# Kernel optimization log

Measured on AMD Instinct MI355X. Metric: run time of the kernel, lower is better.

The kernel has to match this reference:

```python
import jax, jax.numpy as jnp
import numpy as np

IN_FEATURES = 256
EMBED = 512
HEADS = 8
HEAD_DIM = EMBED // HEADS
BLOCKS = 2
FFN = 2048
CLASSES = 1000
NWIRES = 8
BATCH = 8
SEQ = 2048


def _posenc(seq, dim, dtype):
    pos = jnp.arange(seq, dtype=jnp.float32)[:, None]
    div = jnp.exp(jnp.arange(0, dim, 2, dtype=jnp.float32) * (-jnp.log(10000.0) / dim))
    pe = jnp.zeros((seq, dim), dtype=jnp.float32)
    pe = pe.at[:, 0::2].set(jnp.sin(pos * div))
    pe = pe.at[:, 1::2].set(jnp.cos(pos * div))
    return pe.astype(dtype)


def _layer_norm(x, g, b, eps=1e-5):
    mu = jnp.mean(x, axis=-1, keepdims=True)
    var = jnp.var(x, axis=-1, keepdims=True)
    return (x - mu) * jax.lax.rsqrt(var + eps) * g + b


def setup_inputs() -> dict:
    key = jax.random.key(0)
    ks = jax.random.split(key, 20)
    s = 0.02
    inp = {
        'x': jax.random.normal(ks[0], (BATCH, SEQ, IN_FEATURES), dtype=jnp.float32),
        'Wi': jax.random.normal(ks[1], (EMBED, IN_FEATURES), dtype=jnp.float32) * s,
        'bi': jnp.zeros((EMBED,), dtype=jnp.float32),
        'theta_a': jax.random.normal(ks[2], (BLOCKS, NWIRES), dtype=jnp.float32),
        'Wproj': jax.random.normal(ks[3], (BLOCKS, EMBED, NWIRES), dtype=jnp.float32) * s,
        'Wq': jax.random.normal(ks[4], (BLOCKS, EMBED, EMBED), dtype=jnp.float32) * s,
        'Wk': jax.random.normal(ks[5], (BLOCKS, EMBED, EMBED), dtype=jnp.float32) * s,
        'Wv': jax.random.normal(ks[6], (BLOCKS, EMBED, EMBED), dtype=jnp.float32) * s,
        'Wo': jax.random.normal(ks[7], (BLOCKS, EMBED, EMBED), dtype=jnp.float32) * s,
        'g1': jnp.ones((BLOCKS, EMBED), dtype=jnp.float32),
        'b1': jnp.zeros((BLOCKS, EMBED), dtype=jnp.float32),
        'phi': jax.random.normal(ks[8], (BLOCKS, NWIRES), dtype=jnp.float32),
        'W1': jax.random.normal(ks[9], (BLOCKS, FFN, NWIRES), dtype=jnp.float32) * s,
        'W2': jax.random.normal(ks[10], (BLOCKS, EMBED, FFN), dtype=jnp.float32) * s,
        'g2': jnp.ones((BLOCKS, EMBED), dtype=jnp.float32),
        'b2': jnp.zeros((BLOCKS, EMBED), dtype=jnp.float32),
        'Wc': jax.random.normal(ks[11], (CLASSES, EMBED), dtype=jnp.float32) * s,
        'bc': jnp.zeros((CLASSES,), dtype=jnp.float32),
    }
    return inp


def reference(x, Wi, bi, theta_a, Wproj, Wq, Wk, Wv, Wo, g1, b1, phi, W1, W2, g2, b2, Wc, bc):
    b, s, _ = x.shape
    h = jnp.einsum('bsf,ef->bse', x, Wi) + bi          # input_proj
    h = h + _posenc(s, EMBED, h.dtype)[None]           # positional encoding
    scale = 1.0 / np.sqrt(HEAD_DIM)
    for l in range(BLOCKS):
        # --- quantum attention sublayer ---
        # RX encode first NWIRES features + trainable RX per wire -> <Z> = cos(x + theta)
        q_out = jnp.cos(h[..., :NWIRES] + theta_a[l])  # [b,s,nw]
        x_q = jnp.einsum('bsw,ew->bse', q_out, Wproj[l])
        q = jnp.einsum('bse,fe->bsf', x_q, Wq[l]).reshape(b, s, HEADS, HEAD_DIM).transpose(0, 2, 1, 3)
        k = jnp.einsum('bse,fe->bsf', x_q, Wk[l]).reshape(b, s, HEADS, HEAD_DIM).transpose(0, 2, 1, 3)
        v = jnp.einsum('bse,fe->bsf', x_q, Wv[l]).reshape(b, s, HEADS, HEAD_DIM).transpose(0, 2, 1, 3)
        scores = jnp.einsum('bhqd,bhkd->bhqk', q, k) * scale
        attn = jax.nn.softmax(scores, axis=-1)
        out = jnp.einsum('bhqk,bhkd->bhqd', attn, v)
        out = out.transpose(0, 2, 1, 3).reshape(b, s, EMBED)
        attn_out = jnp.einsum('bse,fe->bsf', out, Wo[l])
        h = _layer_norm(h + attn_out, g1[l], b1[l])
        # --- quantum feed-forward sublayer ---
        # RY encode + trainable RY per wire -> <Z> = cos(x + phi)
        qf = jnp.cos(h[..., :NWIRES] + phi[l])         # [b,s,nw]
        f = jnp.einsum('bsw,fw->bsf', qf, W1[l])       # nw -> ffn
        f = jnp.einsum('bsf,ef->bse', jax.nn.relu(f), W2[l])
        h = _layer_norm(h + f, g2[l], b2[l])
    pooled = jnp.mean(h, axis=1)                        # [b, embed]
    logits = jnp.einsum('be,ce->bc', pooled, Wc) + bc
    return logits
```

## Files before the change

### kernel.cpp

```cpp
#include <hip/hip_runtime.h>
#include <hip/hip_bf16.h>
#include <math.h>

#define B_   8
#define S_   2048
#define T_   (B_*S_)
#define FIN  256
#define E_   512
#define H_   8
#define D_   64
#define FFN_ 2048
#define NC_  1000
#define NW_  8

typedef __attribute__((ext_vector_type(8))) short short8;
typedef __attribute__((ext_vector_type(4))) short short4v;
typedef __attribute__((ext_vector_type(4))) float f32x4;
typedef __attribute__((ext_vector_type(2))) unsigned int uint2v;
typedef __attribute__((ext_vector_type(4))) unsigned int uint4v;

__device__ __forceinline__ unsigned short f2bf(float f) {
    __hip_bfloat16 h = __float2bfloat16(f);
    return __builtin_bit_cast(unsigned short, h);
}
__device__ __forceinline__ float bf2f(unsigned short u) {
    return __builtin_bit_cast(float, (unsigned int)u << 16);
}

__device__ __forceinline__ unsigned cvtpk_bf16(float lo, float hi) {
    unsigned r;
    asm("v_cvt_pk_bf16_f32 %0, %1, %2" : "=v"(r) : "v"(lo), "v"(hi));
    return r;
}

#if defined(__has_builtin)
#if __has_builtin(__builtin_amdgcn_permlane32_swap) && __has_builtin(__builtin_amdgcn_permlane16_swap)
#define HAVE_PLSWAP 1
#endif
#endif

__device__ __forceinline__ void lswap32(unsigned &a, unsigned &b) {
#if defined(HAVE_PLSWAP)
    uint2v t = __builtin_amdgcn_permlane32_swap(a, b, false, false);
    a = t[0]; b = t[1];
#else
    unsigned as = (unsigned)__shfl_xor((int)a, 32);
    unsigned bs = (unsigned)__shfl_xor((int)b, 32);
    bool hi = (threadIdx.x & 32) != 0;
    unsigned na = hi ? bs : a;
    unsigned nb = hi ? b  : as;
    a = na; b = nb;
#endif
}
__device__ __forceinline__ void lswap16(unsigned &a, unsigned &b) {
#if defined(HAVE_PLSWAP)
    uint2v t = __builtin_amdgcn_permlane16_swap(a, b, false, false);
    a = t[0]; b = t[1];
#else
    unsigned as = (unsigned)__shfl_xor((int)a, 16);
    unsigned bs = (unsigned)__shfl_xor((int)b, 16);
    bool hi = (threadIdx.x & 16) != 0;
    unsigned na = hi ? bs : a;
    unsigned nb = hi ? b  : as;
    a = na; b = nb;
#endif
}

__device__ __forceinline__ void gld16(void* l, const void* g) {
    __builtin_amdgcn_global_load_lds(
        (const __attribute__((address_space(1))) unsigned int*)g,
        (__attribute__((address_space(3))) unsigned int*)l,
        16, 0, 0);
}

#if defined(__has_builtin)
#if __has_builtin(__builtin_amdgcn_mfma_f32_16x16x16bf16_1k)
#define HAVE_MFMA16 1
#endif
#endif

__device__ __forceinline__ f32x4 mfma16(short4v a, short4v b, f32x4 c) {
#ifdef HAVE_MFMA16
    return __builtin_amdgcn_mfma_f32_16x16x16bf16_1k(a, b, c, 0, 0, 0);
#else
    short8 a8 = {a[0], a[1], a[2], a[3], 0, 0, 0, 0};
    short8 b8 = {b[0], b[1], b[2], b[3], 0, 0, 0, 0};
    return __builtin_amdgcn_mfma_f32_16x16x32_bf16(a8, b8, c, 0, 0, 0);
#endif
}

__global__ __launch_bounds__(256)
void cvt_all(const float* __restrict__ x,  const float* __restrict__ Wi,
             const float* __restrict__ Wo, const float* __restrict__ W2,
             const float* __restrict__ W1,
             unsigned short* xb, unsigned short* Wib,
             unsigned short* Wob, unsigned short* W2b, unsigned short* W1b)
{
    int g = blockIdx.x*256 + threadIdx.x;
    const float* s; unsigned short* d; int o;
    if      (g < 1048576) { s = x;  d = xb;  o = g; }
    else if (g < 1081344) { s = Wi; d = Wib; o = g - 1048576; }
    else if (g < 1212416) { s = Wo; d = Wob; o = g - 1081344; }
    else if (g < 1736704) { s = W2; d = W2b; o = g - 1212416; }
    else                  { s = W1; d = W1b; o = g - 1736704; }
    float4 vv = ((const float4*)s)[o];
    ushort4 u;
    u.x = f2bf(vv.x); u.y = f2bf(vv.y); u.z = f2bf(vv.z); u.w = f2bf(vv.w);
    ((ushort4*)d)[o] = u;
}

__global__ __launch_bounds__(64)
void weff_kernel(const float* __restrict__ Wq, const float* __restrict__ Wk,
                 const float* __restrict__ Wv, const float* __restrict__ Wproj,
                 unsigned short* __restrict__ Weff)
{
    const int f = blockIdx.x, l = blockIdx.y, which = blockIdx.z;
    const int lane = threadIdx.x;
    const float* W = (which == 0 ? Wq : which == 1 ? Wk : Wv)
                     + (size_t)l*E_*E_ + (size_t)f*E_;
    const float* P = Wproj + (size_t)l*E_*NW_;
    const int wv = lane & 7;
    float s = 0.f;
    for (int e = (lane >> 3)*64; e < (lane >> 3)*64 + 64; e++)
        s += W[e] * P[e*NW_ + wv];
    #pragma unroll
    for (int off = 8; off < 64; off <<= 1) s += __shfl_xor(s, off);
    const float scale = (which == 0) ? 0.18033688011112042f : 1.f;
    if (lane < 8)
        Weff[((size_t)(which*2 + l)*E_ + f)*NW_ + lane] = f2bf(s * scale);
}

__global__ __launch_bounds__(64)
void gram_kernel(const unsigned short* __restrict__ Weff, unsigned short* __restrict__ G)
{
    const int hh = blockIdx.x, l = blockIdx.y;
    const int lane = threadIdx.x;
    const int w = lane >> 3, wp = lane & 7;
    const unsigned short* Wq_e = Weff + (size_t)(0*2 + l)*E_*NW_ + (size_t)hh*64*NW_;
    const unsigned short* Wk_e = Weff + (size_t)(1*2 + l)*E_*NW_ + (size_t)hh*64*NW_;
    float s = 0.f;
    for (int d = 0; d < 64; d++)
        s += bf2f(Wq_e[d*NW_ + w]) * bf2f(Wk_e[d*NW_ + wp]);
    G[(size_t)(l*8 + hh)*64 + w*8 + wp] = f2bf(s);
}

__global__ __launch_bounds__(64)
void wov_kernel(const float* __restrict__ Wo, const unsigned short* __restrict__ Weff,
                unsigned short* __restrict__ WoV)
{
    const int f = blockIdx.x, l = blockIdx.y;
    const int lane = threadIdx.x;
    const int hh = lane >> 3, w = lane & 7;
    const float* wrow = Wo + (size_t)l*E_*E_ + (size_t)f*E_ + hh*64;
    const unsigned short* Wv_e = Weff + (size_t)(2*2 + l)*E_*NW_ + (size_t)hh*64*NW_;
    float s = 0.f;
    for (int d = 0; d < 64; d++)
        s += wrow[d] * bf2f(Wv_e[d*NW_ + w]);
    WoV[(size_t)(l*E_ + f)*64 + lane] = f2bf(s);
}

__global__ __launch_bounds__(256)
void qc_small(const unsigned short* __restrict__ h, const float* __restrict__ theta,
              const unsigned short* __restrict__ G,
              unsigned short* __restrict__ c8, unsigned short* __restrict__ c8T,
              unsigned short* __restrict__ gkb)
{
    const int tid = threadIdx.x;
    const int t0 = blockIdx.x * 32;
    __shared__ float cs[32][8];
    __shared__ float Gs[512];
    {
        int tl = tid >> 3, wv2 = tid & 7;
        cs[tl][wv2] = cosf(bf2f(h[(size_t)(t0 + tl)*E_ + wv2]) + theta[wv2]);
        Gs[tid]       = bf2f(G[tid]);
        Gs[tid + 256] = bf2f(G[tid + 256]);
    }
    __syncthreads();
    const int tl = tid >> 3, hh = tid & 7;
    const int bb = (t0 + tl) >> 11, ss = (t0 + tl) & (S_ - 1);
    float c[8];
    #pragma unroll
    for (int i = 0; i < 8; i++) c[i] = cs[tl][i];
    unsigned short u[8] __attribute__((aligned(16)));
    #pragma unroll
    for (int w = 0; w < 8; w++) {
        float s = 0.f;
        #pragma unroll
        for (int wp = 0; wp < 8; wp++) s += Gs[hh*64 + w*8 + wp] * c[wp];
        u[w] = f2bf(s);
    }
    *(float4*)&gkb[((size_t)(bb*H_ + hh)*S_ + ss)*8] = *(float4*)u;
    if (tid < 32) {
        unsigned short v[8] __attribute__((aligned(16)));
        #pragma unroll
        for (int i = 0; i < 8; i++) v[i] = f2bf(cs[tid][i]);
        *(float4*)&c8[(size_t)(t0 + tid)*8] = *(float4*)v;
    } else if (tid < 40) {
        int w = tid - 32;
        unsigned short v[32] __attribute__((aligned(16)));
        #pragma unroll
        for (int s = 0; s < 32; s++) v[s] = f2bf(cs[s][w]);
        unsigned short* dst = c8T + ((size_t)(t0 >> 11)*8 + w)*S_ + (t0 & (S_ - 1));
        #pragma unroll
        for (int cq = 0; cq < 4; cq++) *(float4*)(dst + cq*8) = *(float4*)&v[cq*8];
    }
}

template<int TC_BF16, int MODE>
__global__ __launch_bounds__(256)
void gemm_mfma(const unsigned short* __restrict__ A,
               const unsigned short* __restrict__ Bm,
               void* __restrict__ Cv, int M, int N, int K,
               float scale, const float* __restrict__ bias)
{
    __shared__ char Lraw[32768];
    unsigned short* Al = (unsigned short*)Lraw;
    unsigned short* Bl = (unsigned short*)(Lraw + 16384);
    float* Ot = (float*)Lraw;

    const int tid  = threadIdx.x;
    const int lane = tid & 63;
    const int w    = tid >> 6;
    const int wx   = w & 1, wy = w >> 1;
    int bx, by;
    {
        int nx = gridDim.x;
        int bid = blockIdx.y * nx + blockIdx.x;
        int rpx = gridDim.y >> 3;
        int xcd = bid & 7, idx = bid >> 3;
        by = xcd * rpx + idx / nx;
        bx = idx % nx;
    }
    const int rowBase = by * 128;
    const int colBase = bx * 128;
    const int l15  = lane & 15;
    const int quad = lane >> 4;
    const int srow = lane >> 2;
    const int gch  = (lane & 3) ^ ((srow >> 1) & 3);
    const int swz  = (l15 >> 1) & 3;

    f32x4 acc[4][4] = {};

    #pragma unroll
    for (int it = 0; it < 2; it++) {
        int rb = it*64 + w*16;
        gld16(&Al[rb*32], A  + (size_t)(rowBase + rb + srow)*K + gch*8);
        gld16(&Bl[rb*32], Bm + (size_t)(colBase + rb + srow)*K + gch*8);
    }

    for (int k0 = 0; k0 < K; k0 += 32) {
        const int cur = (k0 >> 5) & 1;
        __syncthreads();
        if (k0 + 32 < K) {
            #pragma unroll
            for (int it = 0; it < 2; it++) {
                int rb = it*64 + w*16;
                gld16(&Al[(1-cur)*4096 + rb*32], A  + (size_t)(rowBase + rb + srow)*K + k0 + 32 + gch*8);
                gld16(&Bl[(1-cur)*4096 + rb*32], Bm + (size_t)(colBase + rb + srow)*K + k0 + 32 + gch*8);
            }
        }
        short8 af[4], bfr[4];
        #pragma unroll
        for (int mi = 0; mi < 4; mi++)
            af[mi] = *(const short8*)&Al[cur*4096 + (wy*64 + mi*16 + l15)*32 + ((quad ^ swz) << 3)];
        #pragma unroll
        for (int ni = 0; ni < 4; ni++)
            bfr[ni] = *(const short8*)&Bl[cur*4096 + (wx*64 + ni*16 + l15)*32 + ((quad ^ swz) << 3)];
        #pragma unroll
        for (int mi = 0; mi < 4; mi++)
            #pragma unroll
            for (int ni = 0; ni < 4; ni++)
                acc[mi][ni] = __builtin_amdgcn_mfma_f32_16x16x32_bf16(
                    af[mi], bfr[ni], acc[mi][ni], 0, 0, 0);
    }

    #pragma unroll
    for (int mi = 0; mi < 4; mi++) {
        __syncthreads();
        #pragma unroll
        for (int ni = 0; ni < 4; ni++) {
            #pragma unroll
            for (int r = 0; r < 4; r++) {
                float v = acc[mi][ni][r] * scale;
                if (MODE == 1) {
                    int row = rowBase + wy*64 + mi*16 + quad*4 + r;
                    int col = colBase + wx*64 + ni*16 + l15;
                    int s = row & (S_ - 1);
                    float freq = __expf(-0.017988946039244957f * (float)(col & ~1));
                    float ang = (float)s * freq;
                    v += bias[col] + ((col & 1) ? cosf(ang) : sinf(ang));
                }
                Ot[(wy*16 + quad*4 + r)*132 + wx*64 + ni*16 + l15] = v;
            }
        }
        __syncthreads();
        {
            int rl = tid >> 3, c0 = (tid & 7) * 16;
            int grow = rowBase + (rl >> 4)*64 + mi*16 + (rl & 15);
            float vv[16];
            #pragma unroll
            for (int j = 0; j < 4; j++)
                *(float4*)&vv[j*4] = *(const float4*)&Ot[rl*132 + c0 + j*4];
            if (TC_BF16) {
                unsigned short u[16] __attribute__((aligned(16)));
                #pragma unroll
                for (int i = 0; i < 16; i++) u[i] = f2bf(vv[i]);
                unsigned short* dst = (unsigned short*)Cv + (size_t)grow*N + colBase + c0;
                *(float4*)dst       = *(float4*)&u[0];
                *(float4*)(dst + 8) = *(float4*)&u[8];
            } else {
                float* dst = (float*)Cv + (size_t)grow*N + colBase + c0;
                #pragma unroll
                for (int j = 0; j < 4; j++)
                    *(float4*)(dst + j*4) = *(const float4*)&vv[j*4];
            }
        }
    }
}

__global__ __launch_bounds__(256)
void gemm_w2f(const unsigned short* __restrict__ h, const float* __restrict__ phi,
              const unsigned short* __restrict__ W1b,
              const unsigned short* __restrict__ W2b,
              unsigned short* __restrict__ tmp)
{
    __shared__ char Lraw[17408];
    unsigned short* Wl = (unsigned short*)Lraw;
    float* Ot = (float*)Lraw;

    const int tid  = threadIdx.x;
    const int lane = tid & 63;
    const int w    = tid >> 6;
    const int tx   = w & 1, ty = w >> 1;
    const int l15  = lane & 15;
    const int quad = lane >> 4;
    const int srow = lane >> 2;
    const int gch  = (lane & 3) ^ ((srow >> 1) & 3);
    const int swz  = (l15 >> 1) & 3;

    const int bid = blockIdx.x;
    const int xcd = bid & 7;
    const int eb  = xcd >> 1;
    const int tb  = (xcd & 1) * 64 + (bid >> 3);
    const int tBase = tb * 128;
    const int eBase = eb * 128;

    short4v cosfr[4];
    #pragma unroll
    for (int nt = 0; nt < 4; nt++) {
        short4v c = {0,0,0,0};
        if (quad < 2) {
            int tok = tBase + ty*64 + nt*16 + l15;
            #pragma unroll
            for (int i = 0; i < 4; i++) {
                int wv = quad*4 + i;
                c[i] = (short)f2bf(cosf(bf2f(h[(size_t)tok*E_ + wv]) + phi[wv]));
            }
        }
        cosfr[nt] = c;
    }

    #pragma unroll
    for (int it = 0; it < 2; it++) {
        int rb = w*32 + it*16;
        gld16(&Wl[rb*32], W2b + (size_t)(eBase + rb + srow)*FFN_ + gch*8);
    }

    const f32x4 fzero = {0.f, 0.f, 0.f, 0.f};
    short4v w1fA[2] = {{0,0,0,0},{0,0,0,0}};

    auto ffn1_pack = [&](short8* pfr_out) {
        unsigned Pm[4][4];
        #pragma unroll
        for (int nt = 0; nt < 4; nt++) {
            #pragma unroll
            for (int jb = 0; jb < 2; jb++) {
                f32x4 c = mfma16(w1fA[jb], cosfr[nt], fzero);
                Pm[nt][jb*2]   = cvtpk_bf16(fmaxf(c[0], 0.f), fmaxf(c[1], 0.f));
                Pm[nt][jb*2+1] = cvtpk_bf16(fmaxf(c[2], 0.f), fmaxf(c[3], 0.f));
            }
            lswap32(Pm[nt][0], Pm[nt][2]); lswap32(Pm[nt][1], Pm[nt][3]);
            lswap16(Pm[nt][0], Pm[nt][2]); lswap16(Pm[nt][1], Pm[nt][3]);
            uint4v u = { Pm[nt][0], Pm[nt][1], Pm[nt][2], Pm[nt][3] };
            pfr_out[nt] = __builtin_bit_cast(short8, u);
        }
    };
    auto load_w1f = [&](int k0) {
        #pragma unroll
        for (int jb = 0; jb < 2; jb++)
            if (quad < 2)
                w1fA[jb] = *(const short4v*)&W1b[(size_t)(k0 + jb*16 + l15)*NW_ + quad*4];
    };

    load_w1f(0);
    short8 pf_cur[4], pf_next[4];
    ffn1_pack(pf_cur);
    load_w1f(32);

    f32x4 acc[4][4] = {};

    for (int k0 = 0; k0 < FFN_; k0 += 32) {
        const int cur = (k0 >> 5) & 1;
        __syncthreads();
        if (k0 + 32 < FFN_) {
            #pragma unroll
            for (int it = 0; it < 2; it++) {
                int rb = w*32 + it*16;
                gld16(&Wl[(1-cur)*4096 + rb*32],
                      W2b + (size_t)(eBase + rb + srow)*FFN_ + k0 + 32 + gch*8);
            }
            ffn1_pack(pf_next);
            if (k0 + 64 < FFN_) load_w1f(k0 + 64);
        }
        #pragma unroll
        for (int et = 0; et < 4; et++) {
            short8 wf = *(const short8*)&Wl[cur*4096 + (tx*64 + et*16 + l15)*32
                                             + ((quad ^ swz) << 3)];
            #pragma unroll
            for (int nt = 0; nt < 4; nt++)
                acc[et][nt] = __builtin_amdgcn_mfma_f32_16x16x32_bf16(
                    wf, pf_cur[nt], acc[et][nt], 0, 0, 0);
        }
        #pragma unroll
        for (int nt = 0; nt < 4; nt++) pf_cur[nt] = pf_next[nt];
    }

    #pragma unroll
    for (int et = 0; et < 4; et++) {
        __syncthreads();
        #pragma unroll
        for (int nt = 0; nt < 4; nt++)
            #pragma unroll
            for (int r = 0; r < 4; r++)
                Ot[(ty*64 + nt*16 + l15)*33 + tx*16 + quad*4 + r] = acc[et][nt][r];
        __syncthreads();
        int token = tid >> 1, half = tid & 1;
        unsigned short u[16] __attribute__((aligned(16)));
        #pragma unroll
        for (int i = 0; i < 16; i++) u[i] = f2bf(Ot[token*33 + half*16 + i]);
        unsigned short* dst = tmp + (size_t)(tBase + token)*E_ + eBase + half*64 + et*16;
        *(float4*)dst       = *(float4*)&u[0];
        *(float4*)(dst + 8) = *(float4*)&u[8];
    }
}

__global__ __launch_bounds__(256)
void flash_q(const unsigned short* __restrict__ c8,
             const unsigned short* __restrict__ c8T,
             const unsigned short* __restrict__ gkb,
             unsigned short* __restrict__ yout)
{
    const int tid  = threadIdx.x;
    const int lane = tid & 63;
    const int wv   = tid >> 6;
    const int l15  = lane & 15;
    const int quad = lane >> 4;
    const int bid  = blockIdx.x;
    const int xcd  = bid & 7;
    const int rest = bid >> 3;
    const int combo = xcd * 8 + (rest >> 4);
    const int qt = rest & 15;
    const int hh = combo & 7;
    const int bb = combo >> 3;
    const size_t qrow0 = (size_t)bb*S_ + (size_t)qt*128;
    const unsigned short* gkp  = gkb + (size_t)(bb*H_ + hh)*S_*NW_;
    const unsigned short* c8Tp = c8T + (size_t)bb*8*S_;

    short4v cqfr[2] = {{0,0,0,0},{0,0,0,0}};
    if (quad < 2) {
        #pragma unroll
        for (int mi = 0; mi < 2; mi++)
            cqfr[mi] = *(const short4v*)&c8[(qrow0 + wv*32 + mi*16 + l15)*NW_ + quad*4];
    }
    const short8 ones8 = {(short)0x3F80, (short)0x3F80, (short)0x3F80, (short)0x3F80,
                          (short)0x3F80, (short)0x3F80, (short)0x3F80, (short)0x3F80};
    f32x4 y[2] = {};

    for (int kt = 0; kt < S_/64; kt++) {
        f32x4 Sc[2][4] = {};
        #pragma unroll
        for (int nt = 0; nt < 4; nt++) {
            short4v gkf = {0,0,0,0};
            if (quad < 2)
                gkf = *(const short4v*)&gkp[(size_t)(kt*64 + nt*16 + l15)*NW_ + quad*4];
            Sc[0][nt] = mfma16(gkf, cqfr[0], Sc[0][nt]);
            Sc[1][nt] = mfma16(gkf, cqfr[1], Sc[1][nt]);
        }
        unsigned Pm[2][8];
        #pragma unroll
        for (int mi = 0; mi < 2; mi++)
            #pragma unroll
            for (int nt = 0; nt < 4; nt++) {
                float e0 = __builtin_amdgcn_exp2f(Sc[mi][nt][0]);
                float e1 = __builtin_amdgcn_exp2f(Sc[mi][nt][1]);
                float e2 = __builtin_amdgcn_exp2f(Sc[mi][nt][2]);
                float e3 = __builtin_amdgcn_exp2f(Sc[mi][nt][3]);
                Pm[mi][nt*2]   = cvtpk_bf16(e0, e1);
                Pm[mi][nt*2+1] = cvtpk_bf16(e2, e3);
            }
        #pragma unroll
        for (int mi = 0; mi < 2; mi++) {
            lswap32(Pm[mi][0], Pm[mi][2]); lswap32(Pm[mi][1], Pm[mi][3]);
            lswap32(Pm[mi][4], Pm[mi][6]); lswap32(Pm[mi][5], Pm[mi][7]);
            lswap16(Pm[mi][0], Pm[mi][2]); lswap16(Pm[mi][1], Pm[mi][3]);
            lswap16(Pm[mi][4], Pm[mi][6]); lswap16(Pm[mi][5], Pm[mi][7]);
        }
        short8 pf[2][2];
        #pragma unroll
        for (int mi = 0; mi < 2; mi++)
            #pragma unroll
            for (int kb = 0; kb < 2; kb++) {
                uint4v u = { Pm[mi][kb*4], Pm[mi][kb*4+1], Pm[mi][kb*4+2], Pm[mi][kb*4+3] };
                pf[mi][kb] = __builtin_bit_cast(short8, u);
            }
        #pragma unroll
        for (int kb = 0; kb < 2; kb++) {
            short8 a8 = {0,0,0,0,0,0,0,0};
            if (l15 < 8)
                a8 = *(const short8*)&c8Tp[(size_t)l15*S_ + kt*64 + kb*32 + quad*8];
            else if (l15 == 8)
                a8 = ones8;
            y[0] = __builtin_amdgcn_mfma_f32_16x16x32_bf16(a8, pf[0][kb], y[0], 0, 0, 0);
            y[1] = __builtin_amdgcn_mfma_f32_16x16x32_bf16(a8, pf[1][kb], y[1], 0, 0, 0);
        }
    }

    #pragma unroll
    for (int mi = 0; mi < 2; mi++) {
        float rs = __shfl(y[mi][0], 32 + l15);
        float inv = 1.f / rs;
        if (quad < 2) {
            unsigned d0 = cvtpk_bf16(y[mi][0]*inv, y[mi][1]*inv);
            unsigned d1 = cvtpk_bf16(y[mi][2]*inv, y[mi][3]*inv);
            unsigned* dst = (unsigned*)&yout[(qrow0 + wv*32 + mi*16 + l15)*64 + hh*8 + quad*4];
            dst[0] = d0; dst[1] = d1;
        }
    }
}

__global__ __launch_bounds__(256)
void add_ln(unsigned short* __restrict__ h, const unsigned short* __restrict__ delta,
            const float* __restrict__ g, const float* __restrict__ b)
{
    const int lane = threadIdx.x & 63;
    const int t = blockIdx.x*4 + (threadIdx.x >> 6);
    const size_t base = (size_t)t*E_ + lane*8;
    uint4 hv = *(const uint4*)&h[base];
    uint4 dv = *(const uint4*)&delta[base];
    float x[8];
    #pragma unroll
    for (int i = 0; i < 4; i++) {
        unsigned hu = ((const unsigned*)&hv)[i], du = ((const unsigned*)&dv)[i];
        x[2*i]   = bf2f((unsigned short)(hu & 0xffff)) + bf2f((unsigned short)(du & 0xffff));
        x[2*i+1] = bf2f((unsigned short)(hu >> 16))    + bf2f((unsigned short)(du >> 16));
    }
    float s = 0.f, sq = 0.f;
    #pragma unroll
    for (int i = 0; i < 8; i++) { s += x[i]; sq += x[i]*x[i]; }
    #pragma unroll
    for (int off = 1; off < 64; off <<= 1) {
        s  += __shfl_xor(s,  off);
        sq += __shfl_xor(sq, off);
    }
    float mu  = s * (1.f/E_);
    float var = sq * (1.f/E_) - mu*mu;
    float rstd = rsqrtf(var + 1e-5f);
    float4 g0 = *(const float4*)&g[lane*8], g1 = *(const float4*)&g[lane*8 + 4];
    float4 b0 = *(const float4*)&b[lane*8], b1 = *(const float4*)&b[lane*8 + 4];
    float gg[8] = {g0.x,g0.y,g0.z,g0.w,g1.x,g1.y,g1.z,g1.w};
    float bb[8] = {b0.x,b0.y,b0.z,b0.w,b1.x,b1.y,b1.z,b1.w};
    uint4 ov;
    #pragma unroll
    for (int i = 0; i < 4; i++) {
        unsigned lo = f2bf((x[2*i]   - mu)*rstd*gg[2*i]   + bb[2*i]);
        unsigned hi = f2bf((x[2*i+1] - mu)*rstd*gg[2*i+1] + bb[2*i+1]);
        ((unsigned*)&ov)[i] = lo | (hi << 16);
    }
    *(uint4*)&h[base] = ov;
}

__global__ __launch_bounds__(256)
void pool_partial(const unsigned short* __restrict__ h, float* __restrict__ part)
{
    const int chunk = blockIdx.x, bb = blockIdx.y, tid = threadIdx.x;
    for (int e = tid; e < E_; e += 256) {
        const unsigned short* p = h + ((size_t)bb*S_ + (size_t)chunk*128)*E_ + e;
        float s = 0.f;
        for (int r = 0; r < 128; r++) s += bf2f(p[(size_t)r*E_]);
        part[(size_t)(bb*16 + chunk)*E_ + e] = s;
    }
}

__global__ __launch_bounds__(256)
void pool_final(const float* __restrict__ part, float* __restrict__ pooled)
{
    const int bb = blockIdx.x, tid = threadIdx.x;
    for (int e = tid; e < E_; e += 256) {
        float s = 0.f;
        #pragma unroll
        for (int c = 0; c < 16; c++) s += part[(size_t)(bb*16 + c)*E_ + e];
        pooled[bb*E_ + e] = s * (1.f/S_);
    }
}

__global__ __launch_bounds__(64)
void classify(const float* __restrict__ pooled, const float* __restrict__ Wc,
              const float* __restrict__ bc, float* __restrict__ out)
{
    const int c = blockIdx.x, bb = blockIdx.y, lane = threadIdx.x;
    const float* p = pooled + bb*E_;
    const float* wc = Wc + (size_t)c*E_;
    float s = 0.f;
    for (int e = lane; e < E_; e += 64) s += p[e]*wc[e];
    #pragma unroll
    for (int off = 1; off < 64; off <<= 1) s += __shfl_xor(s, off);
    if (lane == 0) out[bb*NC_ + c] = s + bc[c];
}

extern "C" void kernel_launch(void* const* d_in, const int* in_sizes, int n_in,
                              void* d_out, int out_size, void* d_ws, size_t ws_size,
                              hipStream_t stream)
{
    const float* x       = (const float*)d_in[0];
    const float* Wi      = (const float*)d_in[1];
    const float* bi      = (const float*)d_in[2];
    const float* theta_a = (const float*)d_in[3];
    const float* Wproj   = (const float*)d_in[4];
    const float* Wq      = (const float*)d_in[5];
    const float* Wk      = (const float*)d_in[6];
    const float* Wv      = (const float*)d_in[7];
    const float* Wo      = (const float*)d_in[8];
    const float* g1      = (const float*)d_in[9];
    const float* b1      = (const float*)d_in[10];
    const float* phi     = (const float*)d_in[11];
    const float* W1      = (const float*)d_in[12];
    const float* W2      = (const float*)d_in[13];
    const float* g2      = (const float*)d_in[14];
    const float* b2      = (const float*)d_in[15];
    const float* Wc      = (const float*)d_in[16];
    const float* bc      = (const float*)d_in[17];
    float* out = (float*)d_out;

    char* ws = (char*)d_ws;
    const size_t MB = 1024u*1024u;
    unsigned short* h      = (unsigned short*)(ws + 0*MB);
    unsigned short* tmp    = (unsigned short*)(ws + 16*MB);
    unsigned short* c8     = (unsigned short*)(ws + 32*MB);
    unsigned short* c8T    = (unsigned short*)(ws + 33*MB);
    unsigned short* gkb    = (unsigned short*)(ws + 34*MB);
    unsigned short* yout   = (unsigned short*)(ws + 48*MB);
    unsigned short* xb     = (unsigned short*)(ws + 96*MB);
    unsigned short* Wib    = (unsigned short*)(ws + 104*MB);
    unsigned short* Wob    = (unsigned short*)(ws + 105*MB);
    unsigned short* W2b    = (unsigned short*)(ws + 106*MB);
    unsigned short* W1b    = (unsigned short*)(ws + 110*MB);
    unsigned short* Weff   = (unsigned short*)(ws + 111*MB);
    unsigned short* Gbuf   = (unsigned short*)(ws + 111*MB + 64*1024);
    unsigned short* WoV    = (unsigned short*)(ws + 111*MB + 128*1024);
    float*          part   = (float*)(ws + 112*MB);
    float*          pooled = (float*)(ws + 112*MB + 512*1024);

    cvt_all<<<6816, 256, 0, stream>>>(x, Wi, Wo, W2, W1, xb, Wib, Wob, W2b, W1b);
    weff_kernel<<<dim3(E_, 2, 3), 64, 0, stream>>>(Wq, Wk, Wv, Wproj, Weff);
    gram_kernel<<<dim3(H_, 2), 64, 0, stream>>>(Weff, Gbuf);
    wov_kernel<<<dim3(E_, 2), 64, 0, stream>>>(Wo, Weff, WoV);

    gemm_mfma<1,1><<<dim3(E_/128, T_/128), 256, 0, stream>>>(
        xb, Wib, h, T_, E_, FIN, 1.f, bi);

    for (int l = 0; l < 2; l++) {
        qc_small<<<T_/32, 256, 0, stream>>>(h, theta_a + l*NW_, Gbuf + (size_t)l*512,
                                            c8, c8T, gkb);
        flash_q<<<(S_/128)*H_*B_, 256, 0, stream>>>(c8, c8T, gkb, yout);
        gemm_mfma<1,0><<<dim3(E_/128, T_/128), 256, 0, stream>>>(
            yout, WoV + (size_t)l*E_*64, tmp, T_, E_, 64, 1.f, nullptr);
        add_ln<<<T_/4, 256, 0, stream>>>(h, tmp, g1 + l*E_, b1 + l*E_);

        gemm_w2f<<<512, 256, 0, stream>>>(h, phi + l*NW_,
                                          W1b + (size_t)l*FFN_*NW_,
                                          W2b + (size_t)l*E_*FFN_, tmp);
        add_ln<<<T_/4, 256, 0, stream>>>(h, tmp, g2 + l*E_, b2 + l*E_);
    }

    pool_partial<<<dim3(16, B_), 256, 0, stream>>>(h, part);
    pool_final<<<B_, 256, 0, stream>>>(part, pooled);
    classify<<<dim3(NC_, B_), 64, 0, stream>>>(pooled, Wc, bc, out);
}
```

Before: 579.2 us.

## Fuse Wo projection with residual LayerNorm and halve gemm_w2f token tile

Adds a wo_ln kernel that computes the K=64 Wo GEMM for 32 tokens with MFMA, stages the result in shared memory, and applies the residual add plus LayerNorm in place on h. This removes the separate gemm_mfma launch, the tmp round-trip through global memory and one add_ln launch per layer. Separately, gemm_w2f now uses 64-token tiles instead of 128, which doubles the grid to 1024 blocks for better occupancy at the cost of reloading W2 twice as often.

```diff
diff --git a/kernel.cpp b/kernel.cpp
--- a/kernel.cpp
+++ b/kernel.cpp
@@ -319,6 +319,86 @@
 }
 
 __global__ __launch_bounds__(256)
+void wo_ln(const unsigned short* __restrict__ yout,
+           const unsigned short* __restrict__ WoV,
+           unsigned short* __restrict__ h,
+           const float* __restrict__ g, const float* __restrict__ b)
+{
+    __shared__ float Ot[16*520];
+    const int tid  = threadIdx.x;
+    const int lane = tid & 63;
+    const int w    = tid >> 6;
+    const int l15  = lane & 15;
+    const int quad = lane >> 4;
+    const size_t t0 = (size_t)blockIdx.x * 32;
+
+    short8 af[2][2];
+    #pragma unroll
+    for (int mi = 0; mi < 2; mi++)
+        #pragma unroll
+        for (int kb = 0; kb < 2; kb++)
+            af[mi][kb] = *(const short8*)&yout[(t0 + mi*16 + l15)*64 + kb*32 + quad*8];
+
+    f32x4 acc[2][8] = {};
+    #pragma unroll
+    for (int ni = 0; ni < 8; ni++)
+        #pragma unroll
+        for (int kb = 0; kb < 2; kb++) {
+            short8 bf8 = *(const short8*)&WoV[(size_t)(w*128 + ni*16 + l15)*64 + kb*32 + quad*8];
+            acc[0][ni] = __builtin_amdgcn_mfma_f32_16x16x32_bf16(af[0][kb], bf8, acc[0][ni], 0, 0, 0);
+            acc[1][ni] = __builtin_amdgcn_mfma_f32_16x16x32_bf16(af[1][kb], bf8, acc[1][ni], 0, 0, 0);
+        }
+
+    #pragma unroll
+    for (int p = 0; p < 2; p++) {
+        __syncthreads();
+        #pragma unroll
+        for (int ni = 0; ni < 8; ni++)
+            #pragma unroll
+            for (int r = 0; r < 4; r++)
+                Ot[(quad*4 + r)*520 + w*128 + ni*16 + l15] = acc[p][ni][r];
+        __syncthreads();
+        const int tk = tid >> 4, u = tid & 15;
+        const size_t trow = t0 + p*16 + tk;
+        float x[32];
+        float s = 0.f, sq = 0.f;
+        #pragma unroll
+        for (int j = 0; j < 8; j++) {
+            int c = u*4 + j*64;
+            ushort4 hv = *(const ushort4*)&h[trow*E_ + c];
+            float4 at = *(const float4*)&Ot[tk*520 + c];
+            float v0 = bf2f(hv.x) + at.x;
+            float v1 = bf2f(hv.y) + at.y;
+            float v2 = bf2f(hv.z) + at.z;
+            float v3 = bf2f(hv.w) + at.w;
+            x[j*4+0] = v0; x[j*4+1] = v1; x[j*4+2] = v2; x[j*4+3] = v3;
+            s  += v0 + v1 + v2 + v3;
+            sq += v0*v0 + v1*v1 + v2*v2 + v3*v3;
+        }
+        #pragma unroll
+        for (int off = 1; off < 16; off <<= 1) {
+            s  += __shfl_xor(s,  off);
+            sq += __shfl_xor(sq, off);
+        }
+        float mu   = s * (1.f/E_);
+        float var  = sq * (1.f/E_) - mu*mu;
+        float rstd = rsqrtf(var + 1e-5f);
+        #pragma unroll
+        for (int j = 0; j < 8; j++) {
+            int c = u*4 + j*64;
+            float4 gv = *(const float4*)&g[c];
+            float4 bv = *(const float4*)&b[c];
+            ushort4 ov;
+            ov.x = f2bf((x[j*4+0] - mu)*rstd*gv.x + bv.x);
+            ov.y = f2bf((x[j*4+1] - mu)*rstd*gv.y + bv.y);
+            ov.z = f2bf((x[j*4+2] - mu)*rstd*gv.z + bv.z);
+            ov.w = f2bf((x[j*4+3] - mu)*rstd*gv.w + bv.w);
+            *(ushort4*)&h[trow*E_ + c] = ov;
+        }
+    }
+}
+
+__global__ __launch_bounds__(256)
 void gemm_w2f(const unsigned short* __restrict__ h, const float* __restrict__ phi,
               const unsigned short* __restrict__ W1b,
               const unsigned short* __restrict__ W2b,
@@ -341,16 +421,16 @@
     const int bid = blockIdx.x;
     const int xcd = bid & 7;
     const int eb  = xcd >> 1;
-    const int tb  = (xcd & 1) * 64 + (bid >> 3);
-    const int tBase = tb * 128;
+    const int tb  = (xcd & 1) * 128 + (bid >> 3);
+    const int tBase = tb * 64;
     const int eBase = eb * 128;
 
-    short4v cosfr[4];
-    #pragma unroll
-    for (int nt = 0; nt < 4; nt++) {
+    short4v cosfr[2];
+    #pragma unroll
+    for (int nt = 0; nt < 2; nt++) {
         short4v c = {0,0,0,0};
         if (quad < 2) {
-            int tok = tBase + ty*64 + nt*16 + l15;
+            int tok = tBase + ty*32 + nt*16 + l15;
             #pragma unroll
             for (int i = 0; i < 4; i++) {
                 int wv = quad*4 + i;
@@ -370,9 +450,9 @@
     short4v w1fA[2] = {{0,0,0,0},{0,0,0,0}};
 
     auto ffn1_pack = [&](short8* pfr_out) {
-        unsigned Pm[4][4];
-        #pragma unroll
-        for (int nt = 0; nt < 4; nt++) {
+        unsigned Pm[2][4];
+        #pragma unroll
+        for (int nt = 0; nt < 2; nt++) {
             #pragma unroll
             for (int jb = 0; jb < 2; jb++) {
                 f32x4 c = mfma16(w1fA[jb], cosfr[nt], fzero);
@@ -393,11 +473,11 @@
     };
 
     load_w1f(0);
-    short8 pf_cur[4], pf_next[4];
+    short8 pf_cur[2], pf_next[2];
     ffn1_pack(pf_cur);
     load_w1f(32);
 
-    f32x4 acc[4][4] = {};
+    f32x4 acc[4][2] = {};
 
     for (int k0 = 0; k0 < FFN_; k0 += 32) {
         const int cur = (k0 >> 5) & 1;
@@ -417,30 +497,30 @@
             short8 wf = *(const short8*)&Wl[cur*4096 + (tx*64 + et*16 + l15)*32
                                              + ((quad ^ swz) << 3)];
             #pragma unroll
-            for (int nt = 0; nt < 4; nt++)
+            for (int nt = 0; nt < 2; nt++)
                 acc[et][nt] = __builtin_amdgcn_mfma_f32_16x16x32_bf16(
                     wf, pf_cur[nt], acc[et][nt], 0, 0, 0);
         }
         #pragma unroll
-        for (int nt = 0; nt < 4; nt++) pf_cur[nt] = pf_next[nt];
+        for (int nt = 0; nt < 2; nt++) pf_cur[nt] = pf_next[nt];
     }
 
     #pragma unroll
     for (int et = 0; et < 4; et++) {
         __syncthreads();
         #pragma unroll
-        for (int nt = 0; nt < 4; nt++)
+        for (int nt = 0; nt < 2; nt++)
             #pragma unroll
             for (int r = 0; r < 4; r++)
-                Ot[(ty*64 + nt*16 + l15)*33 + tx*16 + quad*4 + r] = acc[et][nt][r];
+                Ot[(ty*32 + nt*16 + l15)*33 + tx*16 + quad*4 + r] = acc[et][nt][r];
         __syncthreads();
-        int token = tid >> 1, half = tid & 1;
-        unsigned short u[16] __attribute__((aligned(16)));
-        #pragma unroll
-        for (int i = 0; i < 16; i++) u[i] = f2bf(Ot[token*33 + half*16 + i]);
-        unsigned short* dst = tmp + (size_t)(tBase + token)*E_ + eBase + half*64 + et*16;
-        *(float4*)dst       = *(float4*)&u[0];
-        *(float4*)(dst + 8) = *(float4*)&u[8];
+        int token = tid >> 2, q4 = tid & 3;
+        unsigned short u[8] __attribute__((aligned(16)));
+        #pragma unroll
+        for (int i = 0; i < 8; i++) u[i] = f2bf(Ot[token*33 + q4*8 + i]);
+        unsigned short* dst = tmp + (size_t)(tBase + token)*E_ + eBase
+                              + (q4 >> 1)*64 + et*16 + (q4 & 1)*8;
+        *(float4*)dst = *(float4*)&u[0];
     }
 }
 
@@ -672,13 +752,12 @@
         qc_small<<<T_/32, 256, 0, stream>>>(h, theta_a + l*NW_, Gbuf + (size_t)l*512,
                                             c8, c8T, gkb);
         flash_q<<<(S_/128)*H_*B_, 256, 0, stream>>>(c8, c8T, gkb, yout);
-        gemm_mfma<1,0><<<dim3(E_/128, T_/128), 256, 0, stream>>>(
-            yout, WoV + (size_t)l*E_*64, tmp, T_, E_, 64, 1.f, nullptr);
-        add_ln<<<T_/4, 256, 0, stream>>>(h, tmp, g1 + l*E_, b1 + l*E_);
-
-        gemm_w2f<<<512, 256, 0, stream>>>(h, phi + l*NW_,
-                                          W1b + (size_t)l*FFN_*NW_,
-                                          W2b + (size_t)l*E_*FFN_, tmp);
+        wo_ln<<<T_/32, 256, 0, stream>>>(yout, WoV + (size_t)l*E_*64, h,
+                                         g1 + l*E_, b1 + l*E_);
+
+        gemm_w2f<<<1024, 256, 0, stream>>>(h, phi + l*NW_,
+                                           W1b + (size_t)l*FFN_*NW_,
+                                           W2b + (size_t)l*E_*FFN_, tmp);
         add_ln<<<T_/4, 256, 0, stream>>>(h, tmp, g2 + l*E_, b2 + l*E_);
     }
 
```

Result: faster. 560.6 us (-3.2%).
